# Optimization experiments

Measured on AMD Instinct MI355X. Metric: run time of the kernel, lower is better.

Reference implementation:

```python
import jax, jax.numpy as jnp
import numpy as np
from jax import lax

# ---- model/config constants (from EVL.__init__ with voxel_meters = 0.1) ----
B, C_IN, G = 2, 64, 64          # batch, neck_final channels, voxel grid side
HID = 128                        # head_hidden_dim
NUM_CLASS = 34                   # efm3d taxonomy size
BBOX_MIN, BBOX_MAX = 0.1, 6.0
VOXEL_M = 0.1
OFFSET_MAX = 2.0 * VOXEL_M       # self.offset_max
YAW_MAX = 1.6
DET_THRESH = 0.2
SPLAT_SIGMA = max(1, int(0.12 / VOXEL_M))   # = 1
NMS_RADIUS = SPLAT_SIGMA + 1                 # = 2
TOP_K = 128
VE = (-3.2, 3.2, -3.2, 3.2, -3.2, 3.2)       # xmin,xmax,ymin,ymax,zmin,zmax


def conv3d(x, w, b):
    # x: [B,Ci,D,H,W], w: [Co,Ci,kd,kh,kw]
    y = lax.conv_general_dilated(x, w, (1, 1, 1), 'SAME',
                                 dimension_numbers=('NCDHW', 'OIDHW', 'NCDHW'))
    return y + b[None, :, None, None, None]


def head(x, w1, b1, w2, b2, wf, bf):
    # VolumeCNNHead: two 3x3x3 conv+ReLU layers then 1x1x1 projection
    x = jax.nn.relu(conv3d(x, w1, b1))
    x = jax.nn.relu(conv3d(x, w2, b2))
    return conv3d(x, wf, bf)


def maxpool3d(x, r):
    k = 2 * r + 1
    return lax.reduce_window(x, -jnp.inf, lax.max,
                             (1, 1, k, k, k), (1, 1, 1, 1, 1), 'SAME')


def simple_nms3d(scores, nms_radius):
    # SuperPoint-style iterative windowed NMS, 3D.
    zeros = jnp.zeros_like(scores)
    max_mask = scores == maxpool3d(scores, nms_radius)
    for _ in range(2):
        supp = maxpool3d(max_mask.astype(scores.dtype), nms_radius) > 0
        supp_scores = jnp.where(supp, zeros, scores)
        new_max = supp_scores == maxpool3d(supp_scores, nms_radius)
        max_mask = max_mask | (new_max & ~supp)
    return jnp.where(max_mask, scores, zeros)


def voxel2obb(cent_nms, bbox, clas, ve, top_k, thresh):
    # cent_nms: [B,1,D,H,W], bbox: [B,7,D,H,W], clas: [B,C,D,H,W]
    b, _, D, H, W = cent_nms.shape
    flat = cent_nms.reshape(b, -1)
    scores, idx = lax.top_k(flat, top_k)                  # [B,K]
    iz = idx // (H * W)
    iy = (idx // W) % H
    ix = idx % W
    vx = (ve[1] - ve[0]) / W
    vy = (ve[3] - ve[2]) / H
    vz = (ve[5] - ve[4]) / D
    cx = ve[0] + (ix.astype(jnp.float32) + 0.5) * vx
    cy = ve[2] + (iy.astype(jnp.float32) + 0.5) * vy
    cz = ve[4] + (iz.astype(jnp.float32) + 0.5) * vz
    vox_center = jnp.stack([cx, cy, cz], axis=-1)          # [B,K,3]
    bb = jnp.take_along_axis(bbox.reshape(b, 7, -1), idx[:, None, :], axis=2)  # [B,7,K]
    bb = jnp.transpose(bb, (0, 2, 1))                      # [B,K,7]
    sizes = bb[..., 0:3]
    center = vox_center + bb[..., 3:6]
    yaw = bb[..., 6:7]
    valid = (scores > thresh).astype(scores.dtype)         # [B,K]
    dets = jnp.concatenate([center, sizes, yaw,
                            scores[..., None], valid[..., None]], axis=-1)  # [B,K,9]
    dets = dets * valid[..., None]  # emulate threshold filtering with padding
    cp = jnp.take_along_axis(clas.reshape(b, clas.shape[1], -1),
                             idx[:, None, :], axis=2)      # [B,C,K]
    cp = jnp.transpose(cp, (0, 2, 1)) * valid[..., None]   # [B,K,C]
    return jnp.concatenate([dets, cp], axis=-1)            # [B,K,9+C]


def setup_inputs() -> dict:
    key = jax.random.key(0)
    ks = jax.random.split(key, 16)
    inp = {'neck_feats': jax.random.normal(ks[0], (B, C_IN, G, G, G), jnp.float32)}
    i = 1
    for name, fdim, fbias in [('cent', 1, -5.0), ('bbox', 7, 0.0), ('clas', NUM_CLASS, 0.0)]:
        inp[f'{name}_w1'] = jax.random.normal(ks[i], (HID, C_IN, 3, 3, 3), jnp.float32) / np.float32(np.sqrt(C_IN * 27)); i += 1
        inp[f'{name}_b1'] = jnp.zeros((HID,), jnp.float32)
        inp[f'{name}_w2'] = jax.random.normal(ks[i], (HID, HID, 3, 3, 3), jnp.float32) / np.float32(np.sqrt(HID * 27)); i += 1
        inp[f'{name}_b2'] = jnp.zeros((HID,), jnp.float32)
        inp[f'{name}_wf'] = jax.random.normal(ks[i], (fdim, HID, 1, 1, 1), jnp.float32) / np.float32(np.sqrt(HID)); i += 1
        inp[f'{name}_bf'] = jnp.full((fdim,), fbias, jnp.float32)
    return inp


def reference(neck_feats,
              cent_w1, cent_b1, cent_w2, cent_b2, cent_wf, cent_bf,
              bbox_w1, bbox_b1, bbox_w2, bbox_b2, bbox_wf, bbox_bf,
              clas_w1, clas_b1, clas_w2, clas_b2, clas_wf, clas_bf):
    # heads
    cent_pr = jax.nn.sigmoid(head(neck_feats, cent_w1, cent_b1, cent_w2, cent_b2, cent_wf, cent_bf))
    bbox_raw = head(neck_feats, bbox_w1, bbox_b1, bbox_w2, bbox_b2, bbox_wf, bbox_bf)
    # bbox decode: sizes in [bbox_min, bbox_max], offsets in [-offset_max, offset_max], yaw in [-yaw_max, yaw_max]
    sizes = (BBOX_MAX - BBOX_MIN) * jax.nn.sigmoid(bbox_raw[:, 0:3]) + BBOX_MIN
    offs = OFFSET_MAX * jnp.tanh(bbox_raw[:, 3:6])
    yaw = YAW_MAX * jnp.tanh(bbox_raw[:, 6:7])
    bbox_pr = jnp.concatenate([sizes, offs, yaw], axis=1)   # [B,7,D,H,W]
    clas_pr = jax.nn.softmax(head(neck_feats, clas_w1, clas_b1, clas_w2, clas_b2, clas_wf, clas_bf), axis=1)
    # post_process
    cent_nms = simple_nms3d(cent_pr, NMS_RADIUS)
    dets = voxel2obb(cent_nms, bbox_pr, clas_pr, VE, TOP_K, DET_THRESH)
    return dets  # [B, 128, 9 + NUM_CLASS]
```

## Files before the change

kernel.cpp:

```cpp
#include <hip/hip_runtime.h>
#include <math.h>

#define Gd 64
#define G2 4096
#define G3 262144
#define CIN 64
#define HIDC 128
#define NB 2
#define TOPKN 128
#define NCLASS 34
#define CAPN 65536
#define DET_TH 0.2f

#define NBDATA ((size_t)4096*66*64)
#define TAILB  2048
#define PLANEB ((size_t)64*66*128)
#define ASCALE 16.0f

typedef unsigned char u8;
typedef unsigned short u16;
typedef unsigned int u32;
typedef unsigned long long u64;
typedef int i32x4  __attribute__((ext_vector_type(4)));
typedef int i32x16 __attribute__((ext_vector_type(16)));

__device__ __forceinline__ void glds16(const void* g, void* l){
    __builtin_amdgcn_global_load_lds(
        (const __attribute__((address_space(1))) void*)g,
        (__attribute__((address_space(3))) void*)l, 16, 0, 0);
}

__global__ void wmax_k(const float* __restrict__ w, int n, u32* __restrict__ slot){
    float m = 0.f;
    for (int i = blockIdx.x*256 + threadIdx.x; i < n; i += gridDim.x*256)
        m = fmaxf(m, fabsf(w[i]));
    #pragma unroll
    for (int off=32; off>0; off>>=1)
        m = fmaxf(m, __shfl_xor(m, off));
    if ((threadIdx.x & 63) == 0)
        atomicMax(slot, __float_as_uint(m));
}

__global__ void repack1b_k(const float* __restrict__ w, u8* __restrict__ wq, const u32* __restrict__ slot){
    int i = blockIdx.x*256 + threadIdx.x;
    if (i >= 27*128*64) return;
    float sw = __uint_as_float(*slot) / 127.f;
    int tap = i >> 13;
    int r   = i & 8191;
    int co  = r >> 6;
    int ci  = r & 63;
    float v = w[((size_t)co*64 + ci)*27 + tap];
    int q = (int)rintf(v / sw);
    q = q < -127 ? -127 : (q > 127 ? 127 : q);
    int chunk = ci >> 5, gg = (ci>>4)&1, e = ci&15;
    size_t dst = (((size_t)(tap*2 + chunk)*256 + gg*128 + co))*16 + e;
    wq[dst] = (u8)(signed char)q;
}

__global__ void repack2_k(const float* __restrict__ w, u8* __restrict__ wq, const u32* __restrict__ slot){
    int i = blockIdx.x*256 + threadIdx.x;
    if (i >= 27*128*128) return;
    float sw = __uint_as_float(*slot) / 127.f;
    int tap = i >> 14;
    int r   = i & 16383;
    int co  = r >> 7;
    int ci  = r & 127;
    float v = w[((size_t)co*128 + ci)*27 + tap];
    int q = (int)rintf(v / sw);
    q = q < -127 ? -127 : (q > 127 ? 127 : q);
    int chunk = ci >> 5, gg = (ci>>4)&1, e = ci&15;
    size_t dst = (((size_t)(tap*4 + chunk)*256 + gg*128 + co))*16 + e;
    wq[dst] = (u8)(signed char)q;
}

__global__ void init_k(int* cnt, u32* slots, u8* nbq, u8* h1q, size_t zpoff){
    int t = threadIdx.x;
    if (t < NB) cnt[t]=0;
    if (t < 2)  slots[t]=0;
    for (int e=t; e<TAILB; e+=256){
        nbq[NBDATA+e]=0;
        h1q[zpoff+e]=0;
    }
}

__global__ void __launch_bounds__(256) nbconv_k(const float* __restrict__ in,
                                                u8* __restrict__ nbq){
    const int zy = blockIdx.x;
    const int t  = threadIdx.x;
    __shared__ u8 sh[64][64];
    const int x = t & 63, wv = t >> 6;
    const float* src = in + (size_t)zy*64;
    #pragma unroll
    for (int r=0;r<16;++r){
        int ci = wv*16 + r;
        float a = src[(size_t)ci*G3 + x];
        int q = (int)rintf(a * ASCALE);
        q = q < -127 ? -127 : (q > 127 ? 127 : q);
        sh[x][ci] = (u8)(signed char)q;
    }
    __syncthreads();
    const size_t obase = (size_t)zy*66*64;
    {
        int xx = t >> 2, part = t & 3;
        *(uint4*)(nbq + obase + (size_t)(xx+1)*64 + part*16) = *(const uint4*)&sh[xx][part*16];
    }
    if (t < 32){
        int px = (t<16)?0:65; int off = (t&15)*4;
        *(u32*)(nbq + obase + (size_t)px*64 + off) = 0u;
    }
}

#define ACT_U 3168
#define WG_U  1792

__device__ __forceinline__ void xcd_decode2(int b, int& yt, int& zt){
    int xcd = b & 7, j = b >> 3;
    yt = xcd*2 + (j & 1);
    zt = j >> 1;
}

#define LOADTAP(TAP_, TL_, WV, AV) { \
    int dz_=(TAP_)/9, r9_=(TAP_)-dz_*9, dy_=r9_/3, dx_=r9_-dy_*3; \
    const int wb_ = (TL_)*256 + g*128 + n; \
    _Pragma("unroll") \
    for (int mt_=0; mt_<4; ++mt_) WV[mt_] = wlds[wb_ + mt_*32]; \
    int rowb_ = ((sz+dz_)*6 + (sy+dy_))*66; \
    _Pragma("unroll") \
    for (int j_=0;j_<2;++j_){ \
        int xpos_ = j_*32 + n + dx_; \
        AV[j_] = acth[(rowb_ + xpos_)*2 + (g ^ ((xpos_>>2)&1))]; } }

#define MFMA8(WV, AV) { \
    _Pragma("unroll") \
    for (int j_=0;j_<2;++j_){ \
        i32x4 av_ = *(const i32x4*)&AV[j_]; \
        _Pragma("unroll") \
        for (int mt_=0;mt_<4;++mt_){ \
            i32x4 wv_ = *(const i32x4*)&WV[mt_]; \
            acc[mt_][j_] = __builtin_amdgcn_mfma_i32_32x32x32_i8(wv_, av_, acc[mt_][j_],0,0,0); } } }

#define TAPGROUP(TS_, TC_) { \
    uint4 wvA[4], avA[2], wvB[4], avB[2]; \
    LOADTAP(TS_, 0, wvA, avA); \
    _Pragma("unroll") \
    for (int tl=0; tl<(TC_); ++tl){ \
        if (tl & 1){ \
            if (tl+1 < (TC_)) LOADTAP((TS_)+tl+1, tl+1, wvA, avA); \
            MFMA8(wvB, avB); \
        } else { \
            if (tl+1 < (TC_)) LOADTAP((TS_)+tl+1, tl+1, wvB, avB); \
            MFMA8(wvA, avA); \
        } \
    } }

__global__ void __launch_bounds__(512,2) conv1_mfma(
    const u8* __restrict__ nbq,
    const u8* __restrict__ wq,
    const float* __restrict__ b1, const u32* __restrict__ slot,
    u8* __restrict__ h1q, int z0)
{
    int yt, zt; xcd_decode2(blockIdx.x, yt, zt);
    const int t  = threadIdx.x;
    const int lane = t & 63;
    const int w  = t >> 6;
    const int sz = w >> 2;
    const int sy = w & 3;
    const int n  = lane & 31;
    const int g  = lane >> 5;

    __shared__ uint4 lds[ACT_U + WG_U];
    uint4* acth = lds;
    uint4* wlds = lds + ACT_U;

    const float dq1 = (__uint_as_float(*slot) / 127.f) * (1.0f/ASCALE);

    if (t < 96){
        int row = t>>2, rem = t&3;
        int x = (rem&1)?65:0, s = rem>>1;
        uint4 z; z.x=z.y=z.z=z.w=0u;
        acth[(row*66+x)*2 + s] = z;
    }

    const u8* srcA[6]; int dstA[6];
    #pragma unroll
    for (int p=0;p<6;++p){
        int u = t + p*512;
        int row = u>>7, r = u&127;
        int x = 1 + (r>>1), s = r&1;
        int gg = s ^ ((x>>2)&1);
        int zr = row/6, yr = row - zr*6;
        int zin = z0 - 2 + 2*zt + zr;
        int y   = 4*yt - 1 + yr;
        const u8* a = nbq + NBDATA;
        if ((unsigned)y < 64u && (unsigned)zin < 64u)
            a = nbq + (((size_t)zin*64 + y)*66 + x)*64 + gg*16;
        srcA[p] = a;
        int ub = (t & ~63) + p*512;
        dstA[p] = ub + 4*(ub>>7) + 2;
    }
    const int wq4 = w & 3;
    const int wk0 = w >> 2;

    i32x16 acc[4][2];
    #pragma unroll
    for (int a=0;a<4;++a)
        #pragma unroll
        for (int b2_=0;b2_<2;++b2_)
            #pragma unroll
            for (int r=0;r<16;++r) acc[a][b2_][r]=0;

    for (int c=0; c<2; ++c){
        #pragma unroll
        for (int p=0;p<6;++p)
            glds16(srcA[p] + c*32, &acth[dstA[p]]);
        int ts = 0;
        #pragma unroll
        for (int grp=0; grp<4; ++grp){
            const int tc = (grp<3)?7:6;
            for (int k=wk0; k<tc; k+=2)
                glds16(wq + (((size_t)(ts+k)*2 + c)*256 + wq4*64 + lane)*16,
                       &wlds[k*256 + wq4*64]);
            __syncthreads();
            __builtin_amdgcn_s_setprio(1);
            TAPGROUP(ts, tc)
            __builtin_amdgcn_s_setprio(0);
            __syncthreads();
            ts += tc;
        }
    }

    const int p = 2*zt + sz;
    const int zglob = z0 - 1 + p;
    const int yo = 4*yt + sy;
    const size_t rowbase = ((size_t)p*64 + yo)*66;
    {
        int px = (lane<32)?0:65; int off = (lane&31)*4;
        *(u32*)(h1q + (rowbase + px)*128 + off) = 0u;
    }
    const bool zok = ((unsigned)zglob < 64u);
    #pragma unroll
    for (int mt=0;mt<4;++mt){
        float bvals[16];
        #pragma unroll
        for (int r=0;r<16;++r)
            bvals[r] = b1[mt*32 + (r&3) + 8*(r>>2) + 4*g];
        #pragma unroll
        for (int j=0;j<2;++j){
            size_t base = (rowbase + j*32 + n + 1)*128 + mt*32 + 4*g;
            #pragma unroll
            for (int q=0;q<4;++q){
                u32 packed = 0;
                #pragma unroll
                for (int i=0;i<4;++i){
                    int r = q*4 + i;
                    float v = (float)acc[mt][j][r] * dq1 + bvals[r];
                    v = (zok && v>0.f) ? v : 0.f;
                    int qv = (int)rintf(v * ASCALE);
                    qv = qv > 127 ? 127 : qv;
                    packed |= ((u32)(u8)qv) << (8*i);
                }
                *(u32*)(h1q + base + q*8) = packed;
            }
        }
    }
}

__global__ void __launch_bounds__(512,2) conv2_mfma(
    const u8* __restrict__ h1q,
    const u8* __restrict__ wq,
    const float* __restrict__ b2, const float* __restrict__ wf,
    const float* __restrict__ bf, const u32* __restrict__ slot,
    float* __restrict__ scores, int z0, size_t zpoff)
{
    int yt, zt; xcd_decode2(blockIdx.x, yt, zt);
    const int t  = threadIdx.x;
    const int lane = t & 63;
    const int w  = t >> 6;
    const int sz = w >> 2;
    const int sy = w & 3;
    const int n  = lane & 31;
    const int g  = lane >> 5;

    __shared__ uint4 lds[ACT_U + WG_U];
    uint4* acth = lds;
    uint4* wlds = lds + ACT_U;

    const float dq2 = (__uint_as_float(*slot) / 127.f) * (1.0f/ASCALE);

    if (t < 96){
        int row = t>>2, rem = t&3;
        int x = (rem&1)?65:0, s = rem>>1;
        uint4 z; z.x=z.y=z.z=z.w=0u;
        acth[(row*66+x)*2 + s] = z;
    }

    const u8* srcA[6]; int dstA[6];
    #pragma unroll
    for (int p=0;p<6;++p){
        int u = t + p*512;
        int row = u>>7, r = u&127;
        int x = 1 + (r>>1), s = r&1;
        int gg = s ^ ((x>>2)&1);
        int zr = row/6, yr = row - zr*6;
        int pp = 2*zt + zr;
        int y  = 4*yt - 1 + yr;
        const u8* a = h1q + zpoff;
        if ((unsigned)y < 64u)
            a = h1q + (((size_t)pp*64 + y)*66 + x)*128 + gg*16;
        srcA[p] = a;
        int ub = (t & ~63) + p*512;
        dstA[p] = ub + 4*(ub>>7) + 2;
    }
    const int wq4 = w & 3;
    const int wk0 = w >> 2;

    i32x16 acc[4][2];
    #pragma unroll
    for (int a=0;a<4;++a)
        #pragma unroll
        for (int b2_=0;b2_<2;++b2_)
            #pragma unroll
            for (int r=0;r<16;++r) acc[a][b2_][r]=0;

    for (int c=0; c<4; ++c){
        #pragma unroll
        for (int p=0;p<6;++p)
            glds16(srcA[p] + c*32, &acth[dstA[p]]);
        int ts = 0;
        #pragma unroll
        for (int grp=0; grp<4; ++grp){
            const int tc = (grp<3)?7:6;
            for (int k=wk0; k<tc; k+=2)
                glds16(wq + (((size_t)(ts+k)*4 + c)*256 + wq4*64 + lane)*16,
                       &wlds[k*256 + wq4*64]);
            __syncthreads();
            __builtin_amdgcn_s_setprio(1);
            TAPGROUP(ts, tc)
            __builtin_amdgcn_s_setprio(0);
            __syncthreads();
            ts += tc;
        }
    }

    float part[2] = {0.f, 0.f};
    #pragma unroll
    for (int mt=0;mt<4;++mt){
        #pragma unroll
        for (int r=0;r<16;++r){
            int co = mt*32 + (r&3) + 8*(r>>2) + 4*g;
            float b2v = b2[co], wfv = wf[co];
            #pragma unroll
            for (int j=0;j<2;++j){
                float v = (float)acc[mt][j][r] * dq2 + b2v;
                v = v>0.f?v:0.f;
                part[j] = fmaf(v, wfv, part[j]);
            }
        }
    }
    const int z = z0 + 2*zt + sz;
    const int yo = 4*yt + sy;
    float bfv = bf[0];
    #pragma unroll
    for (int j=0;j<2;++j){
        float tot = part[j] + __shfl_xor(part[j], 32);
        if (g==0)
            scores[((size_t)z*64 + yo)*64 + j*32 + n] = 1.f/(1.f+expf(-(tot+bfv)));
    }
}

__global__ void __launch_bounds__(256) pool_xy_k(const float* __restrict__ in, float* __restrict__ out){
    const int plane = blockIdx.x;
    __shared__ float sp[64][65];
    const float* src = in + (size_t)plane*G2;
    const int t = threadIdx.x;
    for (int e=t; e<4096; e+=256){
        int y=e>>6, x=e&63;
        float v = src[e];
        if (x>=1)  v=fmaxf(v, src[e-1]);
        if (x>=2)  v=fmaxf(v, src[e-2]);
        if (x<=62) v=fmaxf(v, src[e+1]);
        if (x<=61) v=fmaxf(v, src[e+2]);
        sp[y][x]=v;
    }
    __syncthreads();
    float* dst = out + (size_t)plane*G2;
    for (int e=t; e<4096; e+=256){
        int y=e>>6, x=e&63;
        float v = sp[y][x];
        if (y>=1)  v=fmaxf(v, sp[y-1][x]);
        if (y>=2)  v=fmaxf(v, sp[y-2][x]);
        if (y<=62) v=fmaxf(v, sp[y+1][x]);
        if (y<=61) v=fmaxf(v, sp[y+2][x]);
        dst[e]=v;
    }
}

__device__ __forceinline__ float zpool5(const float* __restrict__ a, int i){
    int p = (i >> 12) & 63;
    float v = a[i];
    if (p >= 1)  v = fmaxf(v, a[i - 4096]);
    if (p >= 2)  v = fmaxf(v, a[i - 8192]);
    if (p <= 62) v = fmaxf(v, a[i + 4096]);
    if (p <= 61) v = fmaxf(v, a[i + 8192]);
    return v;
}

__global__ void poolz_eq_k(const float* __restrict__ tA, const float* __restrict__ scores,
                           float* __restrict__ mask){
    int i = blockIdx.x*256 + threadIdx.x;
    if (i >= NB*G3) return;
    mask[i] = (scores[i] == zpool5(tA, i)) ? 1.f : 0.f;
}
__global__ void poolz_supp_k(const float* __restrict__ tA, const float* __restrict__ scores,
                             float* __restrict__ supp, float* __restrict__ ss){
    int i = blockIdx.x*256 + threadIdx.x;
    if (i >= NB*G3) return;
    bool sp = zpool5(tA, i) > 0.f;
    supp[i] = sp ? 1.f : 0.f;
    ss[i]   = sp ? 0.f : scores[i];
}
__global__ void poolz_upd_k(const float* __restrict__ tA, const float* __restrict__ ss,
                            const float* __restrict__ supp, float* __restrict__ mask){
    int i = blockIdx.x*256 + threadIdx.x;
    if (i >= NB*G3) return;
    bool nm = (ss[i] == zpool5(tA, i)) && (supp[i] == 0.f);
    mask[i] = (mask[i] != 0.f || nm) ? 1.f : 0.f;
}

__global__ void compact_k(const float* __restrict__ mask, const float* __restrict__ s,
                          float* __restrict__ lv, int* __restrict__ li, int* __restrict__ cnt){
    int i = blockIdx.x*256 + threadIdx.x;
    if (i >= NB*G3) return;
    if (mask[i]!=0.f && s[i] > DET_TH){
        int b = i >> 18;
        int pos = atomicAdd(&cnt[b],1);
        if (pos < CAPN){
            lv[(size_t)b*CAPN+pos] = s[i];
            li[(size_t)b*CAPN+pos] = i & (G3-1);
        }
    }
}

__device__ __forceinline__ void bitonic2048_desc(u64* sk, int t){
    for (int k=2; k<=2048; k<<=1){
        for (int j=k>>1; j>0; j>>=1){
            #pragma unroll 4
            for (int i=t; i<2048; i+=256){
                int x = i ^ j;
                if (x > i){
                    bool dirDesc = ((i & k) == 0);
                    u64 a = sk[i], b = sk[x];
                    bool sw = dirDesc ? (a < b) : (a > b);
                    if (sw){ sk[i]=b; sk[x]=a; }
                }
            }
            __syncthreads();
        }
    }
}

__global__ void __launch_bounds__(256) topsort_k(const float* __restrict__ lv, const int* __restrict__ li,
                        const int* __restrict__ cnt, float* __restrict__ tv, int* __restrict__ ti){
    const int b = blockIdx.x;
    const int t = threadIdx.x;
    __shared__ u64 sk[2048];
    int n = cnt[b]; if (n > CAPN) n = CAPN;
    const float* Lv = lv + (size_t)b*CAPN;
    const int*   Li = li + (size_t)b*CAPN;

    for (int e=t; e<2048; e+=256){
        u64 key = 0ull;
        if (e < n)
            key = ((u64)__float_as_uint(Lv[e])<<32) | (u32)(~Li[e]);
        sk[e] = key;
    }
    int processed = n < 2048 ? n : 2048;
    __syncthreads();
    bitonic2048_desc(sk, t);
    while (processed < n){
        int chunk = n - processed; if (chunk > 1920) chunk = 1920;
        for (int e=t; e<1920; e+=256){
            u64 key = 0ull;
            if (e < chunk)
                key = ((u64)__float_as_uint(Lv[processed+e])<<32) | (u32)(~Li[processed+e]);
            sk[128+e] = key;
        }
        processed += chunk;
        __syncthreads();
        bitonic2048_desc(sk, t);
    }
    if (t < TOPKN){
        u64 key = sk[t];
        if (key){
            tv[b*TOPKN+t] = __uint_as_float((u32)(key>>32));
            ti[b*TOPKN+t] = (int)(~(u32)key);
        } else {
            tv[b*TOPKN+t] = 0.f;
            ti[b*TOPKN+t] = 0;
        }
    }
}

__global__ void __launch_bounds__(512) perdet_k(
    const float* __restrict__ neck,
    const float* __restrict__ tv, const int* __restrict__ ti,
    const float* __restrict__ bw1, const float* __restrict__ bb1,
    const float* __restrict__ bw2, const float* __restrict__ bb2,
    const float* __restrict__ bwf, const float* __restrict__ bbf,
    const float* __restrict__ lw1, const float* __restrict__ lb1,
    const float* __restrict__ lw2, const float* __restrict__ lb2,
    const float* __restrict__ lwf, const float* __restrict__ lbf,
    float* __restrict__ out)
{
    const int blk = blockIdx.x;
    const int b = blk >> 7, r = blk & 127;
    const int t = threadIdx.x;
    float score = tv[b*TOPKN + r];
    int   idx   = ti[b*TOPKN + r];
    float* orow = out + ((size_t)b*TOPKN + r)*43;
    if (!(score > DET_TH)){
        if (t < 43) orow[t] = 0.f;
        return;
    }
    const int iz = idx >> 12, iy = (idx>>6)&63, ix = idx&63;

    __shared__ float pin[CIN][125];
    __shared__ float h1s[27][HIDC];
    __shared__ float h2s[HIDC];
    __shared__ float raws[7+NCLASS];

    const float* inb = neck + (size_t)b*CIN*G3;
    for (int e=t; e<CIN*125; e+=512){
        int ci=e/125, q=e-ci*125;
        int pz=q/25, py=(q/5)%5, px=q%5;
        int gz=iz-2+pz, gy=iy-2+py, gx=ix-2+px;
        float v=0.f;
        if ((unsigned)gz<64u && (unsigned)gy<64u && (unsigned)gx<64u)
            v = inb[(size_t)ci*G3 + (size_t)gz*G2 + gy*Gd + gx];
        pin[ci][q]=v;
    }
    __syncthreads();

    for (int head=0; head<2; ++head){
        const float* w1 = head? lw1 : bw1;
        const float* b1 = head? lb1 : bb1;
        const float* w2 = head? lw2 : bw2;
        const float* b2 = head? lb2 : bb2;
        const float* wf = head? lwf : bwf;
        const float* bf = head? lbf : bbf;
        const int fdim  = head? NCLASS : 7;

        for (int e=t; e<27*HIDC; e+=512){
            int co = e & 127, pos = e >> 7;
            int pdz=pos/9, pdy=(pos/3)%3, pdx=pos%3;
            int gz=iz-1+pdz, gy=iy-1+pdy, gx=ix-1+pdx;
            float acc = 0.f;
            if ((unsigned)gz<64u && (unsigned)gy<64u && (unsigned)gx<64u){
                acc = b1[co];
                const float* wco = w1 + (size_t)co*CIN*27;
                for (int ci=0; ci<CIN; ++ci){
                    const float* pr = pin[ci];
                    const float* wr = wco + ci*27;
                    #pragma unroll
                    for (int tz=0;tz<3;++tz)
                        #pragma unroll
                        for (int ty=0;ty<3;++ty)
                            #pragma unroll
                            for (int tx=0;tx<3;++tx)
                                acc = fmaf(pr[(pdz+tz)*25+(pdy+ty)*5+(pdx+tx)],
                                           wr[(tz*3+ty)*3+tx], acc);
                }
                acc = acc>0.f ? acc : 0.f;
            }
            h1s[pos][co]=acc;
        }
        __syncthreads();

        if (t < HIDC){
            float acc = b2[t];
            const float* wco = w2 + (size_t)t*HIDC*27;
            for (int pos=0; pos<27; ++pos){
                const float* hr = h1s[pos];
                for (int ci=0; ci<HIDC; ++ci)
                    acc = fmaf(hr[ci], wco[ci*27+pos], acc);
            }
            h2s[t] = acc>0.f ? acc : 0.f;
        }
        __syncthreads();

        if (t < fdim){
            float acc = bf[t];
            const float* wr = wf + t*HIDC;
            for (int ci=0; ci<HIDC; ++ci) acc = fmaf(h2s[ci], wr[ci], acc);
            raws[(head?7:0)+t] = acc;
        }
        __syncthreads();
    }

    if (t==0){
        const float vx = (float)(6.4/64.0);
        float cx = -3.2f + ((float)ix + 0.5f)*vx;
        float cy = -3.2f + ((float)iy + 0.5f)*vx;
        float cz = -3.2f + ((float)iz + 0.5f)*vx;
        float sx = 5.9f*(1.f/(1.f+expf(-raws[0]))) + 0.1f;
        float sy = 5.9f*(1.f/(1.f+expf(-raws[1]))) + 0.1f;
        float sz = 5.9f*(1.f/(1.f+expf(-raws[2]))) + 0.1f;
        float ox = 0.2f*tanhf(raws[3]);
        float oy = 0.2f*tanhf(raws[4]);
        float oz = 0.2f*tanhf(raws[5]);
        float yw = 1.6f*tanhf(raws[6]);
        orow[0]=cx+ox; orow[1]=cy+oy; orow[2]=cz+oz;
        orow[3]=sx; orow[4]=sy; orow[5]=sz;
        orow[6]=yw; orow[7]=score; orow[8]=1.f;
        float mx = raws[7];
        #pragma unroll
        for (int i=1;i<NCLASS;++i) mx = fmaxf(mx, raws[7+i]);
        float ev[NCLASS]; float sum=0.f;
        #pragma unroll
        for (int i=0;i<NCLASS;++i){ ev[i]=expf(raws[7+i]-mx); sum+=ev[i]; }
        float inv = 1.f/sum;
        #pragma unroll
        for (int i=0;i<NCLASS;++i) orow[9+i] = ev[i]*inv;
    }
}

extern "C" void kernel_launch(void* const* d_in, const int* in_sizes, int n_in,
                              void* d_out, int out_size, void* d_ws, size_t ws_size,
                              hipStream_t stream)
{
    (void)in_sizes; (void)n_in; (void)out_size;
    const float* neck = (const float*)d_in[0];
    const float* ce_w1=(const float*)d_in[1],  *ce_b1=(const float*)d_in[2];
    const float* ce_w2=(const float*)d_in[3],  *ce_b2=(const float*)d_in[4];
    const float* ce_wf=(const float*)d_in[5],  *ce_bf=(const float*)d_in[6];
    const float* bb_w1=(const float*)d_in[7],  *bb_b1=(const float*)d_in[8];
    const float* bb_w2=(const float*)d_in[9],  *bb_b2=(const float*)d_in[10];
    const float* bb_wf=(const float*)d_in[11], *bb_bf=(const float*)d_in[12];
    const float* cl_w1=(const float*)d_in[13], *cl_b1=(const float*)d_in[14];
    const float* cl_w2=(const float*)d_in[15], *cl_b2=(const float*)d_in[16];
    const float* cl_wf=(const float*)d_in[17], *cl_bf=(const float*)d_in[18];
    float* out = (float*)d_out;
    char* ws = (char*)d_ws;

    float* scores=(float*)(ws + 0);
    float* tA    =(float*)(ws + (2u<<20));
    float* mask  =(float*)(ws + (8u<<20));
    float* supp  =(float*)(ws + (10u<<20));
    float* ssb   =(float*)(ws + (12u<<20));
    float* lv    =(float*)(ws + (14u<<20));
    int*   li    =(int*)  (ws + (14u<<20) + (512u<<10));
    float* tv    =(float*)(ws + (15u<<20));
    int*   ti    =(int*)  (ws + (15u<<20) + 4096);
    int*   cnt   =(int*)  (ws + (15u<<20) + 8192);
    u32*   slots =(u32*)  (ws + (15u<<20) + 12288);
    u8*    wq1   =(u8*)   (ws + (15u<<20) + 16384);
    u8*    wq2   =(u8*)   (ws + (16u<<20));
    u8*    nbq   =(u8*)   (ws + (17u<<20));
    u8*    h1q   =(u8*)   (ws + (36u<<20));

    const size_t fixedb = 36u<<20;
    int Tz = 4;
    {
        auto need = [&](int nplanes)->size_t{
            return fixedb + (size_t)nplanes*PLANEB + TAILB;
        };
        if      (ws_size >= need(66)) Tz = 64;
        else if (ws_size >= need(34)) Tz = 32;
        else if (ws_size >= need(18)) Tz = 16;
        else if (ws_size >= need(10)) Tz = 8;
    }
    const int nplanes = Tz + 2;
    const size_t zpoff = (size_t)nplanes*PLANEB;

    init_k<<<1, 256, 0, stream>>>(cnt, slots, nbq, h1q, zpoff);
    wmax_k<<<256, 256, 0, stream>>>(ce_w1, 27*128*64,  &slots[0]);
    wmax_k<<<256, 256, 0, stream>>>(ce_w2, 27*128*128, &slots[1]);
    repack1b_k<<<(27*128*64 +255)/256, 256, 0, stream>>>(ce_w1, wq1, &slots[0]);
    repack2_k<<<(27*128*128+255)/256, 256, 0, stream>>>(ce_w2, wq2, &slots[1]);

    for (int b=0; b<NB; ++b){
        const float* inb = neck + (size_t)b*CIN*G3;
        float* scb = scores + (size_t)b*G3;
        nbconv_k<<<4096, 256, 0, stream>>>(inb, nbq);
        for (int z0=0; z0<Gd; z0+=Tz){
            conv1_mfma<<<8*nplanes, 512, 0, stream>>>(nbq, wq1, ce_b1, &slots[0], h1q, z0);
            conv2_mfma<<<8*Tz,      512, 0, stream>>>(h1q, wq2, ce_b2, ce_wf, ce_bf, &slots[1], scb, z0, zpoff);
        }
    }

    const int n = NB*G3, nb = n/256;
    pool_xy_k<<<NB*64,256,0,stream>>>(scores, tA);
    poolz_eq_k<<<nb,256,0,stream>>>(tA, scores, mask);
    for (int it=0; it<2; ++it){
        pool_xy_k<<<NB*64,256,0,stream>>>(mask, tA);
        poolz_supp_k<<<nb,256,0,stream>>>(tA, scores, supp, ssb);
        pool_xy_k<<<NB*64,256,0,stream>>>(ssb, tA);
        poolz_upd_k<<<nb,256,0,stream>>>(tA, ssb, supp, mask);
    }

    compact_k<<<nb,256,0,stream>>>(mask, scores, lv, li, cnt);
    topsort_k<<<NB,256,0,stream>>>(lv, li, cnt, tv, ti);
    perdet_k<<<NB*TOPKN,512,0,stream>>>(neck, tv, ti,
        bb_w1,bb_b1,bb_w2,bb_b2,bb_wf,bb_bf,
        cl_w1,cl_b1,cl_w2,cl_b2,cl_wf,cl_bf, out);
}
```

Before: 573.0 us.

## Stage conv1 output in LDS for coalesced stores and skip padding planes

conv1 now writes its quantized activations into shared memory first, then copies them to global memory as coalesced 16-byte rows, replacing the scattered 4-byte stores. When the whole grid fits in one tile (Tz==64), the always-zero boundary z planes are cleared once by a new kernel, and conv1 launches only over the 64 interior planes instead of 66. This trims conv1 work and improves store efficiency, at the cost of an extra LDS round trip and a sync. It also relies on the workspace being large enough to take the fast path.

```diff
diff --git a/kernel.cpp b/kernel.cpp
--- a/kernel.cpp
+++ b/kernel.cpp
@@ -83,6 +83,15 @@
     }
 }
 
+__global__ void zero_planes_k(u8* __restrict__ h1q, int nplanes){
+    int i = blockIdx.x*256 + threadIdx.x;
+    const int perplane = (int)(PLANEB/16);
+    size_t off = (i < perplane) ? (size_t)i*16
+               : (size_t)(nplanes-1)*PLANEB + (size_t)(i-perplane)*16;
+    uint4 z; z.x=z.y=z.z=z.w=0u;
+    *(uint4*)(h1q + off) = z;
+}
+
 __global__ void __launch_bounds__(256) nbconv_k(const float* __restrict__ in,
                                                 u8* __restrict__ nbq){
     const int zy = blockIdx.x;
@@ -157,7 +166,7 @@
     const u8* __restrict__ nbq,
     const u8* __restrict__ wq,
     const float* __restrict__ b1, const u32* __restrict__ slot,
-    u8* __restrict__ h1q, int z0)
+    u8* __restrict__ h1q, int z0, int pbase)
 {
     int yt, zt; xcd_decode2(blockIdx.x, yt, zt);
     const int t  = threadIdx.x;
@@ -173,6 +182,7 @@
     uint4* wlds = lds + ACT_U;
 
     const float dq1 = (__uint_as_float(*slot) / 127.f) * (1.0f/ASCALE);
+    const int pblk = pbase + 2*zt;
 
     if (t < 96){
         int row = t>>2, rem = t&3;
@@ -189,7 +199,7 @@
         int x = 1 + (r>>1), s = r&1;
         int gg = s ^ ((x>>2)&1);
         int zr = row/6, yr = row - zr*6;
-        int zin = z0 - 2 + 2*zt + zr;
+        int zin = z0 - 2 + pblk + zr;
         int y   = 4*yt - 1 + yr;
         const u8* a = nbq + NBDATA;
         if ((unsigned)y < 64u && (unsigned)zin < 64u)
@@ -229,15 +239,16 @@
         }
     }
 
-    const int p = 2*zt + sz;
+    const int p = pblk + sz;
     const int zglob = z0 - 1 + p;
-    const int yo = 4*yt + sy;
-    const size_t rowbase = ((size_t)p*64 + yo)*66;
-    {
-        int px = (lane<32)?0:65; int off = (lane&31)*4;
-        *(u32*)(h1q + (rowbase + px)*128 + off) = 0u;
-    }
     const bool zok = ((unsigned)zglob < 64u);
+    u32* ols = (u32*)lds;
+    if (t < 256){
+        int row = t>>5, xsel = (t>>4)&1, c4 = (t&15)*2;
+        int pos = row*66 + (xsel?65:0);
+        ols[pos*33 + c4] = 0u;
+        ols[pos*33 + c4 + 1] = 0u;
+    }
     #pragma unroll
     for (int mt=0;mt<4;++mt){
         float bvals[16];
@@ -246,7 +257,7 @@
             bvals[r] = b1[mt*32 + (r&3) + 8*(r>>2) + 4*g];
         #pragma unroll
         for (int j=0;j<2;++j){
-            size_t base = (rowbase + j*32 + n + 1)*128 + mt*32 + 4*g;
+            int pos = w*66 + j*32 + n + 1;
             #pragma unroll
             for (int q=0;q<4;++q){
                 u32 packed = 0;
@@ -259,9 +270,20 @@
                     qv = qv > 127 ? 127 : qv;
                     packed |= ((u32)(u8)qv) << (8*i);
                 }
-                *(u32*)(h1q + base + q*8) = packed;
+                ols[pos*33 + mt*8 + g + 2*q] = packed;
             }
         }
+    }
+    __syncthreads();
+    for (int k=t; k<4224; k+=512){
+        int pos = k>>3, q = k&7;
+        int row = pos/66, x = pos - row*66;
+        int base = pos*33 + q*4;
+        uint4 v;
+        v.x = ols[base+0]; v.y = ols[base+1]; v.z = ols[base+2]; v.w = ols[base+3];
+        int p_  = pblk + (row>>2);
+        int yo_ = 4*yt + (row&3);
+        *(uint4*)(h1q + (((size_t)p_*64 + yo_)*66 + x)*128 + q*16) = v;
     }
 }
 
@@ -671,20 +693,26 @@
     }
     const int nplanes = Tz + 2;
     const size_t zpoff = (size_t)nplanes*PLANEB;
+    const bool fast = (Tz == 64);
 
     init_k<<<1, 256, 0, stream>>>(cnt, slots, nbq, h1q, zpoff);
     wmax_k<<<256, 256, 0, stream>>>(ce_w1, 27*128*64,  &slots[0]);
     wmax_k<<<256, 256, 0, stream>>>(ce_w2, 27*128*128, &slots[1]);
     repack1b_k<<<(27*128*64 +255)/256, 256, 0, stream>>>(ce_w1, wq1, &slots[0]);
     repack2_k<<<(27*128*128+255)/256, 256, 0, stream>>>(ce_w2, wq2, &slots[1]);
+    if (fast)
+        zero_planes_k<<<264, 256, 0, stream>>>(h1q, nplanes);
 
     for (int b=0; b<NB; ++b){
         const float* inb = neck + (size_t)b*CIN*G3;
         float* scb = scores + (size_t)b*G3;
         nbconv_k<<<4096, 256, 0, stream>>>(inb, nbq);
         for (int z0=0; z0<Gd; z0+=Tz){
-            conv1_mfma<<<8*nplanes, 512, 0, stream>>>(nbq, wq1, ce_b1, &slots[0], h1q, z0);
-            conv2_mfma<<<8*Tz,      512, 0, stream>>>(h1q, wq2, ce_b2, ce_wf, ce_bf, &slots[1], scb, z0, zpoff);
+            if (fast)
+                conv1_mfma<<<8*64, 512, 0, stream>>>(nbq, wq1, ce_b1, &slots[0], h1q, z0, 1);
+            else
+                conv1_mfma<<<8*nplanes, 512, 0, stream>>>(nbq, wq1, ce_b1, &slots[0], h1q, z0, 0);
+            conv2_mfma<<<8*Tz, 512, 0, stream>>>(h1q, wq2, ce_b2, ce_wf, ce_bf, &slots[1], scb, z0, zpoff);
         }
     }
 
```

New measurement: 509.3 us. 11.1% less time.
